# Kernel tuning notes

Hardware: AMD Instinct MI355X
Metric: run time of the kernel (lower is better)

Reference implementation:

```python
import jax, jax.numpy as jnp
import numpy as np

B, N, E = 8, 1024, 512
H, D = 8, 64
F = 2048


def setup_inputs() -> dict:
    key = jax.random.key(0)
    ks = jax.random.split(key, 12)
    s = lambda *sh: 1.0 / np.sqrt(sh[-1])
    inp = {
        "input1": jax.random.normal(ks[0], (B, N, E), dtype=jnp.float32),
        # projection weights stored as [in, out] (torch weight transposed)
        "Wq": jax.random.normal(ks[1], (E, H * D), dtype=jnp.float32) * s(E, E),
        "Wk": jax.random.normal(ks[2], (E, H * D), dtype=jnp.float32) * s(E, E),
        "Wv": jax.random.normal(ks[3], (E, H * D), dtype=jnp.float32) * s(E, E),
        "Wo": jax.random.normal(ks[4], (H * D, E), dtype=jnp.float32) * s(E, E),
        "bo": jnp.zeros((E,), dtype=jnp.float32),
        "g1": jnp.ones((E,), dtype=jnp.float32),
        "b1": jnp.zeros((E,), dtype=jnp.float32),
        "W1": jax.random.normal(ks[5], (E, F), dtype=jnp.float32) * s(E, E),
        "bf1": jnp.zeros((F,), dtype=jnp.float32),
        "W2": jax.random.normal(ks[6], (F, E), dtype=jnp.float32) * s(F, F),
        "bf2": jnp.zeros((E,), dtype=jnp.float32),
        "g2": jnp.ones((E,), dtype=jnp.float32),
        "b2": jnp.zeros((E,), dtype=jnp.float32),
    }
    return inp


def _layernorm(x, g, b, eps=1e-5):
    mu = jnp.mean(x, axis=-1, keepdims=True)
    var = jnp.var(x, axis=-1, keepdims=True)
    return (x - mu) * jax.lax.rsqrt(var + eps) * g + b


def reference(input1, Wq, Wk, Wv, Wo, bo, g1, b1, W1, bf1, W2, bf2, g2, b2):
    x = input1
    # QKV projections, split heads: [B, H, N, D]
    q = (x @ Wq).reshape(B, N, H, D).transpose(0, 2, 1, 3)
    k = (x @ Wk).reshape(B, N, H, D).transpose(0, 2, 1, 3)
    v = (x @ Wv).reshape(B, N, H, D).transpose(0, 2, 1, 3)
    # scaled dot-product attention (naive, materialized scores as in source)
    score = jnp.einsum("bhnd,bhmd->bhnm", q, k) / jnp.sqrt(jnp.float32(D))
    weights = jax.nn.softmax(score, axis=-1)
    out = jnp.einsum("bhnm,bhmd->bhnd", weights, v)
    out_concat = out.transpose(0, 2, 1, 3).reshape(B, N, H * D)
    mh = out_concat @ Wo + bo
    out1 = _layernorm(x + mh, g1, b1)
    ff = jax.nn.relu(out1 @ W1 + bf1) @ W2 + bf2
    out3 = _layernorm(out1 + ff, g2, b2)
    return (out3, 0)
```

## Files before the change

### kernel.cpp

```cpp
#include <hip/hip_runtime.h>
#include <cstdint>
#include <cstddef>

typedef _Float16 h8 __attribute__((ext_vector_type(8)));
typedef _Float16 h4 __attribute__((ext_vector_type(4)));
typedef __fp16   g2 __attribute__((ext_vector_type(2)));
typedef float    f32x4 __attribute__((ext_vector_type(4)));

constexpr int B_ = 8, N_ = 1024, E_ = 512, H_ = 8, D_ = 64, F_ = 2048;
constexpr int M_ = B_ * N_;
constexpr int HD_ = H_ * D_;

#define QSCALE2 0.18033688011112042f

#define GLOAD_LDS16(gp, lp)                                                        \
    __builtin_amdgcn_global_load_lds((const __attribute__((address_space(1))) void*)(gp), \
                                     (__attribute__((address_space(3))) void*)(lp), 16, 0, 0)

__global__ void __launch_bounds__(256) k_cvt(const float* __restrict__ in,
                                             _Float16* __restrict__ out, int n) {
    int i = (blockIdx.x * 256 + threadIdx.x) * 4;
    if (i + 3 < n) {
        float4 v = *(const float4*)(in + i);
        h4 o = {(_Float16)v.x, (_Float16)v.y, (_Float16)v.z, (_Float16)v.w};
        *(h4*)(out + i) = o;
    }
}

__global__ void __launch_bounds__(256) k_tr6(
    const float* __restrict__ Wq, const float* __restrict__ Wk,
    const float* __restrict__ Wv, const float* __restrict__ Wo,
    const float* __restrict__ W1, const float* __restrict__ W2,
    _Float16* __restrict__ oqkv, _Float16* __restrict__ oo,
    _Float16* __restrict__ o1, _Float16* __restrict__ o2) {
    const float* in;
    _Float16* out;
    int R, C, gt = blockIdx.x;
    switch (blockIdx.z) {
        case 0: in = Wq; out = oqkv;              R = 512;  C = 512;  break;
        case 1: in = Wk; out = oqkv + 512 * 512;  R = 512;  C = 512;  break;
        case 2: in = Wv; out = oqkv + 1024 * 512; R = 512;  C = 512;  break;
        case 3: in = Wo; out = oo;                R = 512;  C = 512;  break;
        default:
            if (blockIdx.z < 8) { in = W1; out = o1; R = 512;  C = 2048; gt += (blockIdx.z - 4) * 256; }
            else                { in = W2; out = o2; R = 2048; C = 512;  gt += (blockIdx.z - 8) * 256; }
    }
    const int ctiles = C >> 5;
    const int ty = gt / ctiles, tx = gt - ty * ctiles;
    const int r0 = ty * 32, c0 = tx * 32;
    __shared__ float lt[32][33];
    const int rr = threadIdx.x >> 3, cq = threadIdx.x & 7;
    float4 v = *(const float4*)&in[(size_t)(r0 + rr) * C + c0 + cq * 4];
    lt[rr][cq * 4 + 0] = v.x; lt[rr][cq * 4 + 1] = v.y;
    lt[rr][cq * 4 + 2] = v.z; lt[rr][cq * 4 + 3] = v.w;
    __syncthreads();
    h4 o = {(_Float16)lt[cq * 4 + 0][rr], (_Float16)lt[cq * 4 + 1][rr],
            (_Float16)lt[cq * 4 + 2][rr], (_Float16)lt[cq * 4 + 3][rr]};
    *(h4*)&out[(size_t)(c0 + rr) * R + r0 + cq * 4] = o;
}

template <int BN, int EPI>
__global__ void __launch_bounds__(256) k_gemm(
    const _Float16* __restrict__ A, const _Float16* __restrict__ Bt,
    int Mg, int Ng, int Kg,
    const float* __restrict__ bias, const float* __restrict__ res,
    const _Float16* __restrict__ resh, _Float16* __restrict__ outh,
    _Float16* __restrict__ qp, _Float16* __restrict__ kp, _Float16* __restrict__ vtp) {
    constexpr int WN = BN / 2;
    constexpr int NI = WN / 16;
    __shared__ alignas(16) _Float16 lA[2][64 * 64];
    __shared__ alignas(16) _Float16 lB[2][BN * 64];

    const int tid = threadIdx.x;
    const int lane = tid & 63;
    const int wid = tid >> 6;
    const int wr = wid >> 1, wc = wid & 1;
    const int r16 = lane & 15, hseg = lane >> 4;

    const int bid = blockIdx.x;
    const int xcd = bid & 7;
    const int rem = bid >> 3;
    const int tx = rem >> 4, tyl = rem & 15;
    const int m0 = (xcd * 16 + tyl) * 64;
    const int n0 = tx * BN;

    auto STAGE = [&](int buf, int k0) {
#pragma unroll
        for (int i = 0; i < 2; ++i) {
            const int slot = i * 256 + tid, row = slot >> 3;
            const int cs = (slot & 7) ^ (row & 7);
            GLOAD_LDS16(A + (size_t)(m0 + row) * Kg + k0 + cs * 8, &lA[buf][slot * 8]);
        }
#pragma unroll
        for (int i = 0; i < BN / 32; ++i) {
            const int slot = i * 256 + tid, row = slot >> 3;
            const int cs = (slot & 7) ^ (row & 7);
            GLOAD_LDS16(Bt + (size_t)(n0 + row) * Kg + k0 + cs * 8, &lB[buf][slot * 8]);
        }
    };

    f32x4 acc[2][NI] = {};
    const int nt = Kg >> 6;

    STAGE(0, 0);
    __syncthreads();

    for (int t = 0; t < nt; ++t) {
        const int cur = t & 1;
        if (t + 1 < nt) STAGE(cur ^ 1, (t + 1) << 6);

#pragma unroll
        for (int kk = 0; kk < 2; ++kk) {
            h8 af[2], bf[NI];
#pragma unroll
            for (int mi = 0; mi < 2; ++mi) {
                const int row = wr * 32 + mi * 16 + r16;
                af[mi] = *(const h8*)&lA[cur][row * 64 + (((kk * 4 + hseg) ^ (row & 7)) * 8)];
            }
#pragma unroll
            for (int ni = 0; ni < NI; ++ni) {
                const int row = wc * WN + ni * 16 + r16;
                bf[ni] = *(const h8*)&lB[cur][row * 64 + (((kk * 4 + hseg) ^ (row & 7)) * 8)];
            }
#pragma unroll
            for (int mi = 0; mi < 2; ++mi)
#pragma unroll
                for (int ni = 0; ni < NI; ++ni)
                    acc[mi][ni] =
                        __builtin_amdgcn_mfma_f32_16x16x32_f16(af[mi], bf[ni], acc[mi][ni], 0, 0, 0);
        }
        __syncthreads();
    }

    if constexpr (EPI == 0) {
        if (n0 >= 1024) {
            _Float16* lC = &lA[0][0];
#pragma unroll
            for (int mi = 0; mi < 2; ++mi) {
                const int r0 = wr * 32 + mi * 16 + hseg * 4;
                const int s = r0 >> 3, ro = r0 & 7;
#pragma unroll
                for (int ni = 0; ni < NI; ++ni) {
                    const int c = wc * WN + ni * 16 + r16;
                    h4 pv = {(_Float16)acc[mi][ni][0], (_Float16)acc[mi][ni][1],
                             (_Float16)acc[mi][ni][2], (_Float16)acc[mi][ni][3]};
                    *(h4*)&lC[c * 64 + ((s ^ (c & 7)) << 3) + ro] = pv;
                }
            }
            __syncthreads();
            const int c = tid >> 1, half = tid & 1;
            const int b = m0 >> 10, nn0 = m0 & 1023;
            _Float16* gdst =
                vtp + ((size_t)(b * 512 + (n0 - 1024) + c)) * 1024 + nn0 + half * 32;
#pragma unroll
            for (int j = 0; j < 4; ++j) {
                const int s = half * 4 + j;
                h8 v = *(const h8*)&lC[c * 64 + ((s ^ (c & 7)) << 3)];
                *(h8*)&gdst[j * 8] = v;
            }
        } else {
#pragma unroll
            for (int mi = 0; mi < 2; ++mi)
#pragma unroll
                for (int ni = 0; ni < NI; ++ni)
#pragma unroll
                    for (int r = 0; r < 4; ++r) {
                        int row = m0 + wr * 32 + mi * 16 + hseg * 4 + r;
                        int col = n0 + wc * WN + ni * 16 + r16;
                        float v = acc[mi][ni][r];
                        int cc = col & 511;
                        int h = cc >> 6, d = cc & 63;
                        int b = row >> 10, nn = row & 1023;
                        if (col < 512)
                            qp[((b * 8 + h) * 1024 + nn) * 64 + d] = (_Float16)(v * QSCALE2);
                        else
                            kp[((b * 8 + h) * 1024 + nn) * 64 + d] = (_Float16)v;
                    }
        }
    } else {
#pragma unroll
        for (int mi = 0; mi < 2; ++mi)
#pragma unroll
            for (int ni = 0; ni < NI; ++ni)
#pragma unroll
                for (int r = 0; r < 4; ++r) {
                    int row = m0 + wr * 32 + mi * 16 + hseg * 4 + r;
                    int col = n0 + wc * WN + ni * 16 + r16;
                    float v = acc[mi][ni][r] + bias[col];
                    if constexpr (EPI == 1) {
                        v += res[(size_t)row * Ng + col];
                    } else if constexpr (EPI == 3) {
                        v += (float)resh[(size_t)row * Ng + col];
                    } else {
                        v = v > 0.f ? v : 0.f;
                    }
                    outh[(size_t)row * Ng + col] = (_Float16)v;
                }
    }
}

__global__ void __launch_bounds__(256) k_attn(const _Float16* __restrict__ q,
                                              const _Float16* __restrict__ k,
                                              const _Float16* __restrict__ vt,
                                              _Float16* __restrict__ attn) {
    __shared__ alignas(16) _Float16 lK[2][64 * 64];
    __shared__ alignas(16) _Float16 lV[2][64 * 64];
    __shared__ alignas(16) _Float16 lP[4][16 * 64];

    const int tid = threadIdx.x, lane = tid & 63, w = tid >> 6;
    const int bid = blockIdx.x;
    const int xcd = bid & 7, rem = bid >> 3;
    const int bh = xcd * 8 + (rem & 7);
    const int q0 = (rem >> 3) * 64;
    const int r16 = lane & 15, hseg = lane >> 4;
    const size_t base = (size_t)bh * N_ * D_;

    h8 qf0 = *(const h8*)&q[base + (size_t)(q0 + w * 16 + r16) * 64 + hseg * 8];
    h8 qf1 = *(const h8*)&q[base + (size_t)(q0 + w * 16 + r16) * 64 + 32 + hseg * 8];

    int srow[2], scsrc[2];
#pragma unroll
    for (int i = 0; i < 2; ++i) {
        int slot = i * 256 + tid;
        srow[i] = slot >> 3;
        scsrc[i] = (slot & 7) ^ (srow[i] & 7);
    }

    auto STAGE = [&](int buf, int kt) {
#pragma unroll
        for (int i = 0; i < 2; ++i)
            GLOAD_LDS16(k + base + kt * 4096 + srow[i] * 64 + scsrc[i] * 8,
                        &lK[buf][(i * 256 + tid) * 8]);
#pragma unroll
        for (int i = 0; i < 2; ++i)
            GLOAD_LDS16(vt + base + (size_t)srow[i] * N_ + kt * 64 + scsrc[i] * 8,
                        &lV[buf][(i * 256 + tid) * 8]);
    };

    float mrun = -1e30f, lrun = 0.f;
    f32x4 oacc[4] = {};

    const char* lKb = (const char*)&lK[0][0];
    const char* lVb = (const char*)&lV[0][0];
    char* lPb = (char*)&lP[0][0] + w * 2048;
    const int swz = r16 & 7;
    const int kb0 = r16 * 128 + ((hseg ^ swz) * 16);
    const int kb1 = r16 * 128 + (((4 + hseg) ^ swz) * 16);
    const int pswz = swz * 8;
    const int prd0 = r16 * 128 + (((hseg * 8) ^ pswz) * 2);
    const int prd1 = r16 * 128 + (((32 + hseg * 8) ^ pswz) * 2);
    const int pwr0 = r16 * 128 + (((0 + hseg * 4) ^ pswz) * 2);
    const int pwr1 = r16 * 128 + (((16 + hseg * 4) ^ pswz) * 2);
    const int pwr2 = r16 * 128 + (((32 + hseg * 4) ^ pswz) * 2);
    const int pwr3 = r16 * 128 + (((48 + hseg * 4) ^ pswz) * 2);

    auto TILE = [&](const int cur, const int kt) __attribute__((always_inline)) {
        if (kt + 1 < N_ / 64) STAGE(cur ^ 1, kt + 1);
        const int cOff = cur * 8192;

        float sv[4][4];
#pragma unroll
        for (int t4 = 0; t4 < 4; ++t4) {
            f32x4 a = {};
            h8 kf0 = *(const h8*)(lKb + cOff + t4 * 2048 + kb0);
            a = __builtin_amdgcn_mfma_f32_16x16x32_f16(kf0, qf0, a, 0, 0, 0);
            h8 kf1 = *(const h8*)(lKb + cOff + t4 * 2048 + kb1);
            a = __builtin_amdgcn_mfma_f32_16x16x32_f16(kf1, qf1, a, 0, 0, 0);
#pragma unroll
            for (int r = 0; r < 4; ++r) sv[t4][r] = a[r];
        }

        float mx = sv[0][0];
#pragma unroll
        for (int t4 = 0; t4 < 4; ++t4)
#pragma unroll
            for (int r = 0; r < 4; ++r) mx = fmaxf(mx, sv[t4][r]);
        mx = fmaxf(mx, __shfl_xor(mx, 16));
        mx = fmaxf(mx, __shfl_xor(mx, 32));

        if (__any(mx > mrun + 8.f)) {
            float mnew = fmaxf(mrun, mx);
            float sc = exp2f(mrun - mnew);
            mrun = mnew;
            lrun *= sc;
#pragma unroll
            for (int r = 0; r < 4; ++r) {
                float scq = __shfl(sc, hseg * 4 + r);
#pragma unroll
                for (int nf = 0; nf < 4; ++nf) oacc[nf][r] *= scq;
            }
        }

        float p[4][4];
        float rsum = 0.f;
#pragma unroll
        for (int t4 = 0; t4 < 4; ++t4)
#pragma unroll
            for (int r = 0; r < 4; ++r) {
                p[t4][r] = exp2f(sv[t4][r] - mrun);
                rsum += p[t4][r];
            }
        rsum += __shfl_xor(rsum, 16);
        rsum += __shfl_xor(rsum, 32);
        lrun += rsum;

#pragma unroll
        for (int t4 = 0; t4 < 4; ++t4) {
            g2 a0 = __builtin_amdgcn_cvt_pkrtz(p[t4][0], p[t4][1]);
            g2 a1 = __builtin_amdgcn_cvt_pkrtz(p[t4][2], p[t4][3]);
            h4 pv = {(_Float16)a0[0], (_Float16)a0[1], (_Float16)a1[0], (_Float16)a1[1]};
            char* dst = lPb + (t4 == 0 ? pwr0 : t4 == 1 ? pwr1 : t4 == 2 ? pwr2 : pwr3);
            *(h4*)dst = pv;
        }
        asm volatile("s_waitcnt lgkmcnt(0)" ::: "memory");

        h8 pa0 = *(const h8*)(lPb + prd0);
        h8 pa1 = *(const h8*)(lPb + prd1);
#pragma unroll
        for (int nf = 0; nf < 4; ++nf) {
            h8 vb0 = *(const h8*)(lVb + cOff + nf * 2048 + kb0);
            oacc[nf] = __builtin_amdgcn_mfma_f32_16x16x32_f16(pa0, vb0, oacc[nf], 0, 0, 0);
            h8 vb1 = *(const h8*)(lVb + cOff + nf * 2048 + kb1);
            oacc[nf] = __builtin_amdgcn_mfma_f32_16x16x32_f16(pa1, vb1, oacc[nf], 0, 0, 0);
        }
        __syncthreads();
    };

    STAGE(0, 0);
    __syncthreads();

    for (int kt = 0; kt < N_ / 64; kt += 2) {
        TILE(0, kt);
        TILE(1, kt + 1);
    }

    float rlin = 1.f / lrun;
    int b = bh >> 3, h = bh & 7;
#pragma unroll
    for (int r = 0; r < 4; ++r) {
        float inv = __shfl(rlin, hseg * 4 + r);
        int row = b * 1024 + q0 + w * 16 + hseg * 4 + r;
#pragma unroll
        for (int nf = 0; nf < 4; ++nf) {
            int col = h * 64 + nf * 16 + r16;
            attn[(size_t)row * 512 + col] = (_Float16)(oacc[nf][r] * inv);
        }
    }
}

template <int OUTF32>
__global__ void __launch_bounds__(256) k_ln(const _Float16* __restrict__ x,
                                            const float* __restrict__ g,
                                            const float* __restrict__ b,
                                            float* __restrict__ outf,
                                            _Float16* __restrict__ outh,
                                            float* __restrict__ tail) {
    int row = blockIdx.x * 4 + (threadIdx.x >> 6);
    int lane = threadIdx.x & 63;
    h8 v = *(const h8*)(x + (size_t)row * 512 + lane * 8);
    float f[8];
    float s = 0.f, sq = 0.f;
#pragma unroll
    for (int j = 0; j < 8; ++j) {
        f[j] = (float)v[j];
        s += f[j];
        sq += f[j] * f[j];
    }
#pragma unroll
    for (int msk = 1; msk < 64; msk <<= 1) {
        s += __shfl_xor(s, msk);
        sq += __shfl_xor(sq, msk);
    }
    float mu = s * (1.f / 512.f);
    float var = sq * (1.f / 512.f) - mu * mu;
    float rstd = rsqrtf(var + 1e-5f);
    float4 ga = *(const float4*)(g + lane * 8);
    float4 gb = *(const float4*)(g + lane * 8 + 4);
    float4 ba = *(const float4*)(b + lane * 8);
    float4 bb = *(const float4*)(b + lane * 8 + 4);
    float o[8];
    o[0] = (f[0] - mu) * rstd * ga.x + ba.x;
    o[1] = (f[1] - mu) * rstd * ga.y + ba.y;
    o[2] = (f[2] - mu) * rstd * ga.z + ba.z;
    o[3] = (f[3] - mu) * rstd * ga.w + ba.w;
    o[4] = (f[4] - mu) * rstd * gb.x + bb.x;
    o[5] = (f[5] - mu) * rstd * gb.y + bb.y;
    o[6] = (f[6] - mu) * rstd * gb.z + bb.z;
    o[7] = (f[7] - mu) * rstd * gb.w + bb.w;
    if constexpr (OUTF32) {
        float* orow = outf + (size_t)row * 512 + lane * 8;
        *(float4*)(orow) = make_float4(o[0], o[1], o[2], o[3]);
        *(float4*)(orow + 4) = make_float4(o[4], o[5], o[6], o[7]);
        if (tail && blockIdx.x == 0 && threadIdx.x == 0) tail[0] = 0.f;
    } else {
        h8 oh = {(_Float16)o[0], (_Float16)o[1], (_Float16)o[2], (_Float16)o[3],
                 (_Float16)o[4], (_Float16)o[5], (_Float16)o[6], (_Float16)o[7]};
        *(h8*)(outh + (size_t)row * 512 + lane * 8) = oh;
    }
}

extern "C" void kernel_launch(void* const* d_in, const int* in_sizes, int n_in,
                              void* d_out, int out_size, void* d_ws, size_t ws_size,
                              hipStream_t stream) {
    const float* x   = (const float*)d_in[0];
    const float* Wq  = (const float*)d_in[1];
    const float* Wk  = (const float*)d_in[2];
    const float* Wv  = (const float*)d_in[3];
    const float* Wo  = (const float*)d_in[4];
    const float* bo  = (const float*)d_in[5];
    const float* g1  = (const float*)d_in[6];
    const float* b1  = (const float*)d_in[7];
    const float* W1  = (const float*)d_in[8];
    const float* bf1 = (const float*)d_in[9];
    const float* W2  = (const float*)d_in[10];
    const float* bf2 = (const float*)d_in[11];
    const float* g2  = (const float*)d_in[12];
    const float* b2  = (const float*)d_in[13];
    float* out = (float*)d_out;

    char* ws = (char*)d_ws;
    _Float16* xh    = (_Float16*)(ws + 0);
    _Float16* wqkvT = (_Float16*)(ws + 8388608);
    _Float16* woT   = (_Float16*)(ws + 9961472);
    _Float16* w1T   = (_Float16*)(ws + 10485760);
    _Float16* w2T   = (_Float16*)(ws + 12582912);
    _Float16* qb    = (_Float16*)(ws + 14680064);
    _Float16* kb    = (_Float16*)(ws + 23068672);
    _Float16* vtb   = (_Float16*)(ws + 31457280);
    _Float16* attnb = (_Float16*)(ws + 39845888);
    _Float16* h1h   = (_Float16*)(ws + 48234496);
    _Float16* out1h = xh;
    _Float16* ff    = qb;

    k_cvt<<<dim3(M_ * E_ / 1024), 256, 0, stream>>>(x, xh, M_ * E_);
    k_tr6<<<dim3(256, 1, 12), 256, 0, stream>>>(Wq, Wk, Wv, Wo, W1, W2,
                                                wqkvT, woT, w1T, w2T);

    k_gemm<128, 0><<<dim3(1536), 256, 0, stream>>>(
        xh, wqkvT, M_, 1536, 512, nullptr, nullptr, nullptr, nullptr, qb, kb, vtb);

    k_attn<<<dim3(1024), 256, 0, stream>>>(qb, kb, vtb, attnb);

    k_gemm<64, 1><<<dim3(1024), 256, 0, stream>>>(
        attnb, woT, M_, 512, 512, bo, x, nullptr, h1h, nullptr, nullptr, nullptr);

    k_ln<0><<<dim3(M_ / 4), 256, 0, stream>>>(h1h, g1, b1, nullptr, out1h, nullptr);

    k_gemm<128, 2><<<dim3(2048), 256, 0, stream>>>(
        out1h, w1T, M_, 2048, 512, bf1, nullptr, nullptr, ff, nullptr, nullptr, nullptr);

    k_gemm<64, 3><<<dim3(1024), 256, 0, stream>>>(
        ff, w2T, M_, 512, 2048, bf2, nullptr, out1h, h1h, nullptr, nullptr, nullptr);

    k_ln<1><<<dim3(M_ / 4), 256, 0, stream>>>(h1h, g2, b2, out, nullptr, out + (size_t)M_ * E_);
}
```

Baseline: 152.2 us.

## Merge input conversion into weight transpose kernel and streamline attention softmax

Fuses the fp32-to-fp16 input conversion and the six weight transposes into one launch, using 1024x13 blocks where the transpose slices exit early beyond 256 blocks. In the attention inner loop, the max is now reduced across lanes only when a rescale is triggered, and the row-sum cross-lane reduction is deferred to the end. exp2f is replaced by the raw hardware exp instruction, and s_setprio raises wave priority around the MFMA sections. Launching many empty blocks adds some scheduling overhead. The lazy max check now runs on per-lane partial maxima rather than full row maxima, which changes when rescales fire.

```diff
diff --git a/kernel.cpp b/kernel.cpp
--- a/kernel.cpp
+++ b/kernel.cpp
@@ -17,22 +17,34 @@
     __builtin_amdgcn_global_load_lds((const __attribute__((address_space(1))) void*)(gp), \
                                      (__attribute__((address_space(3))) void*)(lp), 16, 0, 0)
 
-__global__ void __launch_bounds__(256) k_cvt(const float* __restrict__ in,
-                                             _Float16* __restrict__ out, int n) {
-    int i = (blockIdx.x * 256 + threadIdx.x) * 4;
-    if (i + 3 < n) {
-        float4 v = *(const float4*)(in + i);
-        h4 o = {(_Float16)v.x, (_Float16)v.y, (_Float16)v.z, (_Float16)v.w};
-        *(h4*)(out + i) = o;
-    }
-}
-
-__global__ void __launch_bounds__(256) k_tr6(
+__device__ __forceinline__ float exp2_raw(float x) {
+#if __has_builtin(__builtin_amdgcn_exp2f)
+    return __builtin_amdgcn_exp2f(x);
+#else
+    float r;
+    asm("v_exp_f32 %0, %1\n\ts_nop 0" : "=v"(r) : "v"(x));
+    return r;
+#endif
+}
+
+__global__ void __launch_bounds__(256) k_pre(
+    const float* __restrict__ x, _Float16* __restrict__ xh,
     const float* __restrict__ Wq, const float* __restrict__ Wk,
     const float* __restrict__ Wv, const float* __restrict__ Wo,
     const float* __restrict__ W1, const float* __restrict__ W2,
     _Float16* __restrict__ oqkv, _Float16* __restrict__ oo,
     _Float16* __restrict__ o1, _Float16* __restrict__ o2) {
+    if (blockIdx.z == 12) {
+        int i = (blockIdx.x * 256 + threadIdx.x) * 16;
+#pragma unroll
+        for (int j = 0; j < 4; ++j) {
+            float4 v = *(const float4*)(x + i + j * 4);
+            h4 o = {(_Float16)v.x, (_Float16)v.y, (_Float16)v.z, (_Float16)v.w};
+            *(h4*)(xh + i + j * 4) = o;
+        }
+        return;
+    }
+    if (blockIdx.x >= 256) return;
     const float* in;
     _Float16* out;
     int R, C, gt = blockIdx.x;
@@ -259,6 +271,7 @@
         const int cOff = cur * 8192;
 
         float sv[4][4];
+        __builtin_amdgcn_s_setprio(1);
 #pragma unroll
         for (int t4 = 0; t4 < 4; ++t4) {
             f32x4 a = {};
@@ -269,18 +282,19 @@
 #pragma unroll
             for (int r = 0; r < 4; ++r) sv[t4][r] = a[r];
         }
-
-        float mx = sv[0][0];
-#pragma unroll
-        for (int t4 = 0; t4 < 4; ++t4)
-#pragma unroll
-            for (int r = 0; r < 4; ++r) mx = fmaxf(mx, sv[t4][r]);
-        mx = fmaxf(mx, __shfl_xor(mx, 16));
-        mx = fmaxf(mx, __shfl_xor(mx, 32));
+        __builtin_amdgcn_s_setprio(0);
+
+        float m0a = fmaxf(fmaxf(sv[0][0], sv[0][1]), fmaxf(sv[0][2], sv[0][3]));
+        float m1a = fmaxf(fmaxf(sv[1][0], sv[1][1]), fmaxf(sv[1][2], sv[1][3]));
+        float m2a = fmaxf(fmaxf(sv[2][0], sv[2][1]), fmaxf(sv[2][2], sv[2][3]));
+        float m3a = fmaxf(fmaxf(sv[3][0], sv[3][1]), fmaxf(sv[3][2], sv[3][3]));
+        float mx = fmaxf(fmaxf(m0a, m1a), fmaxf(m2a, m3a));
 
         if (__any(mx > mrun + 8.f)) {
+            mx = fmaxf(mx, __shfl_xor(mx, 16));
+            mx = fmaxf(mx, __shfl_xor(mx, 32));
             float mnew = fmaxf(mrun, mx);
-            float sc = exp2f(mrun - mnew);
+            float sc = exp2_raw(mrun - mnew);
             mrun = mnew;
             lrun *= sc;
 #pragma unroll
@@ -297,11 +311,9 @@
         for (int t4 = 0; t4 < 4; ++t4)
 #pragma unroll
             for (int r = 0; r < 4; ++r) {
-                p[t4][r] = exp2f(sv[t4][r] - mrun);
+                p[t4][r] = exp2_raw(sv[t4][r] - mrun);
                 rsum += p[t4][r];
             }
-        rsum += __shfl_xor(rsum, 16);
-        rsum += __shfl_xor(rsum, 32);
         lrun += rsum;
 
 #pragma unroll
@@ -316,6 +328,7 @@
 
         h8 pa0 = *(const h8*)(lPb + prd0);
         h8 pa1 = *(const h8*)(lPb + prd1);
+        __builtin_amdgcn_s_setprio(1);
 #pragma unroll
         for (int nf = 0; nf < 4; ++nf) {
             h8 vb0 = *(const h8*)(lVb + cOff + nf * 2048 + kb0);
@@ -323,6 +336,7 @@
             h8 vb1 = *(const h8*)(lVb + cOff + nf * 2048 + kb1);
             oacc[nf] = __builtin_amdgcn_mfma_f32_16x16x32_f16(pa1, vb1, oacc[nf], 0, 0, 0);
         }
+        __builtin_amdgcn_s_setprio(0);
         __syncthreads();
     };
 
@@ -333,6 +347,9 @@
         TILE(0, kt);
         TILE(1, kt + 1);
     }
+
+    lrun += __shfl_xor(lrun, 16);
+    lrun += __shfl_xor(lrun, 32);
 
     float rlin = 1.f / lrun;
     int b = bh >> 3, h = bh & 7;
@@ -432,9 +449,8 @@
     _Float16* out1h = xh;
     _Float16* ff    = qb;
 
-    k_cvt<<<dim3(M_ * E_ / 1024), 256, 0, stream>>>(x, xh, M_ * E_);
-    k_tr6<<<dim3(256, 1, 12), 256, 0, stream>>>(Wq, Wk, Wv, Wo, W1, W2,
-                                                wqkvT, woT, w1T, w2T);
+    k_pre<<<dim3(1024, 1, 13), 256, 0, stream>>>(x, xh, Wq, Wk, Wv, Wo, W1, W2,
+                                                 wqkvT, woT, w1T, w2T);
 
     k_gemm<128, 0><<<dim3(1536), 256, 0, stream>>>(
         xh, wqkvT, M_, 1536, 512, nullptr, nullptr, nullptr, nullptr, qb, kb, vtb);
```

After: 143.5 us. -5.7%, faster.
